# Performance work log

Hardware: AMD Instinct MI355X
Metric: run time of the kernel (lower is better)

The kernel has to match this reference:

```python
import jax, jax.numpy as jnp
import numpy as np
import math

E = 2048; H = 16; NOPE = 128; ROPE = 64; VH = 128; C = 512; QR = 1536
DR = 2; BASE = 10000.0; LR = 4  # hypernet low_rank -> C//4 = 128
B = 2; S = 2048


def _ln(x, g, b):
    m = jnp.mean(x, axis=-1, keepdims=True)
    v = jnp.mean((x - m) ** 2, axis=-1, keepdims=True)
    return (x - m) / jnp.sqrt(v + 1e-5) * g + b


def _rope(x, sin, cos):
    # interleaved rotary: x[..., 0::2], x[..., 1::2]
    x1 = x[..., 0::2]
    x2 = x[..., 1::2]
    out = jnp.stack([x1 * cos - x2 * sin, x1 * sin + x2 * cos], axis=-1)
    return out.reshape(x.shape)


def _sincos(pos, dim):
    inv = BASE ** (-jnp.arange(0, dim, 2, dtype=jnp.float32) / dim)
    ang = pos[:, None] * inv  # [S, dim//2]
    return jnp.sin(ang), jnp.cos(ang)


def _pe(T, d):
    # sinusoidal positional encoding [T, d]
    pos = jnp.arange(T, dtype=jnp.float32)[:, None]
    div = jnp.exp(jnp.arange(0, d, 2, dtype=jnp.float32) * (-math.log(10000.0) / d))
    pe = jnp.zeros((T, d))
    pe = pe.at[:, 0::2].set(jnp.sin(pos * div))
    pe = pe.at[:, 1::2].set(jnp.cos(pos * div))
    return pe


def _forward(query, key, value, wq_a, q_ln_g, q_ln_b, wq_b, wkv_a, kv_ln_g,
             kv_ln_b, wkv_b, wo, fc_c_w, fc_c_b, fc_p_w, fc_p_b, pos_scale):
    B_, S_, _ = query.shape
    # LoRA query path
    ql = _ln(query @ wq_a.T, q_ln_g, q_ln_b)                 # [B,S,QR]
    q = (ql @ wq_b.T).reshape(B_, S_, H, NOPE + ROPE)
    q_nope, q_pe = q[..., :NOPE], q[..., NOPE:]
    # positions: start_pos = key_len - 1 (prefill entering incremental path)
    start = S_ - 1
    pos = jnp.arange(start, start + S_, dtype=jnp.float32)
    sin, cos = _sincos(pos, ROPE)                            # [S, ROPE//2]
    q_pe = _rope(q_pe, sin[None, :, None, :], cos[None, :, None, :])
    # KV latent path
    kvf = key @ wkv_a.T                                      # [B,S,C+ROPE]
    kv, k_pe = kvf[..., :C], kvf[..., C:]
    k_pe = _rope(k_pe, sin[None, :, :], cos[None, :, :])     # [B,S,ROPE]
    kvn = _ln(kv, kv_ln_g, kv_ln_b)                          # [B,S,C]
    # HyperNetwork temporal compression: W [B, t, T]
    T = S_
    t = math.ceil(T / DR)
    Cpe = _pe(t, C)                                          # [t, C]
    C2 = Cpe @ fc_c_w.T + fc_c_b                             # [t, C//LR]
    P2 = kvn @ fc_p_w.T + fc_p_b                             # [B,T,C//LR]
    W = jax.nn.sigmoid(jnp.einsum('tr,bTr->btT', C2, P2))    # [B,t,T]
    # chunk mask: compressed slot r gathers tokens in its down_rate chunk
    zm = (jnp.arange(T)[None, :] // DR == jnp.arange(t)[:, None]).astype(kvn.dtype)
    prev_kv = jnp.einsum('btT,bTc->btc', W * zm[None], kvn)  # [B,t,C]
    idx = list(range(DR - 1, T, DR))
    if T - 1 not in idx:
        idx.append(T - 1)
    prev_kpe = k_pe[:, np.array(idx)]                        # [B,t,ROPE]
    # LoRA-absorbed attention
    wkvb = wkv_b.reshape(H, NOPE + VH, C)
    qn = jnp.einsum('bshd,hdc->bshc', q_nope, wkvb[:, :NOPE])
    content = jnp.einsum('bshc,btc->bsht', qn, prev_kv)
    # decoupled (normalized) rope scores
    qpe_n = q_pe / jnp.maximum(jnp.linalg.norm(q_pe, axis=-1, keepdims=True), 1e-12)
    kpe_n = prev_kpe / jnp.maximum(jnp.linalg.norm(prev_kpe, axis=-1, keepdims=True), 1e-12)
    pscore = jnp.einsum('bshr,btr->bsht', qpe_n, kpe_n)
    scores = (content + pos_scale * pscore) * ((NOPE + ROPE) ** -0.5)
    attn = jax.nn.softmax(scores, axis=-1)                   # [B,S,H,t]
    x = jnp.einsum('bsht,btc->bshc', attn, prev_kv)
    x = jnp.einsum('bshc,hdc->bshd', x, wkvb[:, NOPE:])      # value up-proj
    return x.reshape(B_, S_, H * VH) @ wo.T


def setup_inputs() -> dict:
    key = jax.random.key(0)
    ks = jax.random.split(key, 16)
    s = 0.02
    return {
        'query': jax.random.normal(ks[0], (B, S, E), jnp.float32),
        'key': jax.random.normal(ks[1], (B, S, E), jnp.float32),
        'value': jax.random.normal(ks[2], (B, S, E), jnp.float32),
        'wq_a': jax.random.normal(ks[3], (QR, E), jnp.float32) * s,
        'q_ln_g': jnp.ones((QR,), jnp.float32),
        'q_ln_b': jnp.zeros((QR,), jnp.float32),
        'wq_b': jax.random.normal(ks[4], (H * (NOPE + ROPE), QR), jnp.float32) * s,
        'wkv_a': jax.random.normal(ks[5], (C + ROPE, E), jnp.float32) * s,
        'kv_ln_g': jnp.ones((C,), jnp.float32),
        'kv_ln_b': jnp.zeros((C,), jnp.float32),
        'wkv_b': jax.random.normal(ks[6], (H * (NOPE + VH), C), jnp.float32) * s,
        'wo': jax.random.normal(ks[7], (E, H * VH), jnp.float32) * s,
        'fc_c_w': jax.random.normal(ks[8], (C // LR, C), jnp.float32) * s,
        'fc_c_b': jnp.zeros((C // LR,), jnp.float32),
        'fc_p_w': jax.random.normal(ks[9], (C // LR, C), jnp.float32) * s,
        'fc_p_b': jnp.zeros((C // LR,), jnp.float32),
        'pos_scale': jnp.asarray(1.0, jnp.float32),
    }


def reference(query, key, value, wq_a, q_ln_g, q_ln_b, wq_b, wkv_a, kv_ln_g,
              kv_ln_b, wkv_b, wo, fc_c_w, fc_c_b, fc_p_w, fc_p_b, pos_scale):
    return _forward(query, key, value, wq_a, q_ln_g, q_ln_b, wq_b, wkv_a,
                    kv_ln_g, kv_ln_b, wkv_b, wo, fc_c_w, fc_c_b, fc_p_w,
                    fc_p_b, pos_scale)
```

## Files before the change

### kernel.cpp

```cpp
#include <hip/hip_runtime.h>
#include <math.h>

#define S_ 2048
#define B_ 2
#define H_ 16
#define E_ 2048
#define QR_ 1536
#define NOPE_ 128
#define ROPE_ 64
#define C_ 512
#define VH_ 128
#define T_ 1024
#define LN1E4 9.210340371976184f
#define SCALE_ 0.07216878364870323f

typedef _Float16 half8 __attribute__((ext_vector_type(8)));
typedef _Float16 half4 __attribute__((ext_vector_type(4)));
typedef __fp16 fp16x2 __attribute__((ext_vector_type(2)));
typedef float floatx4 __attribute__((ext_vector_type(4)));
#define MFMA16(a, b, c) __builtin_amdgcn_mfma_f32_16x16x32_f16(a, b, c, 0, 0, 0)

__device__ __forceinline__ void gload16(const _Float16* g, _Float16* l) {
  __builtin_amdgcn_global_load_lds(
      (__attribute__((address_space(1))) const void*)g,
      (__attribute__((address_space(3))) void*)l, 16, 0, 0);
}

__device__ __forceinline__ int xcd_swizzle(int orig, int nwg) {
  int q8 = nwg >> 3, r8 = nwg & 7, xcd = orig & 7, base = orig >> 3;
  return (xcd < r8 ? xcd * (q8 + 1) : r8 * (q8 + 1) + (xcd - r8) * q8) + base;
}

__global__ __launch_bounds__(256) void conv_all(
    const float* __restrict__ q, const float* __restrict__ k,
    const float* __restrict__ wqa, const float* __restrict__ wqb,
    const float* __restrict__ wkva, const float* __restrict__ wo,
    const float* __restrict__ fcc, const float* __restrict__ fcp,
    _Float16* q16, _Float16* k16, _Float16* wqa16, _Float16* wqb16,
    _Float16* wkva16, _Float16* wo16, _Float16* fcc16, _Float16* fcp16)
{
  size_t i = (size_t)blockIdx.x * 256 + threadIdx.x;
  const float* in; _Float16* out; size_t off;
  if      (i < 1048576) { in = q;    out = q16;    off = i; }
  else if (i < 2097152) { in = k;    out = k16;    off = i - 1048576; }
  else if (i < 2490368) { in = wqa;  out = wqa16;  off = i - 2097152; }
  else if (i < 3080192) { in = wqb;  out = wqb16;  off = i - 2490368; }
  else if (i < 3227648) { in = wkva; out = wkva16; off = i - 3080192; }
  else if (i < 3751936) { in = wo;   out = wo16;   off = i - 3227648; }
  else if (i < 3760128) { in = fcc;  out = fcc16;  off = i - 3751936; }
  else                  { in = fcp;  out = fcp16;  off = i - 3760128; }
  float4 a = ((const float4*)in)[2 * off];
  float4 b = ((const float4*)in)[2 * off + 1];
  half8 h = {(_Float16)a.x, (_Float16)a.y, (_Float16)a.z, (_Float16)a.w,
             (_Float16)b.x, (_Float16)b.y, (_Float16)b.z, (_Float16)b.w};
  *(half8*)(out + 8 * off) = h;
}

template<bool OUT16, bool NB, bool BIAS, bool TRANSC>
__global__ __launch_bounds__(256) void gemm16(
    const _Float16* __restrict__ A, const _Float16* __restrict__ Bm,
    const float* __restrict__ bias, float* __restrict__ Cf,
    _Float16* __restrict__ Ch, int N, int K, int lda, int ldb, int ldc,
    long sAb, long sAh, long sBb, long sBh, long sCb, long sCh)
{
  __shared__ __align__(16) _Float16 Asl[2][128 * 64];
  __shared__ __align__(16) _Float16 Bsl[2][128 * 64];
  const int z = blockIdx.z, zb = z >> 4, zh = z & 15;
  A  += (size_t)zb * sAb + (size_t)zh * sAh;
  Bm += (size_t)zb * sBb + (size_t)zh * sBh;
  if (OUT16) Ch += (size_t)zb * sCb + (size_t)zh * sCh;
  else       Cf += (size_t)zb * sCb + (size_t)zh * sCh;
  const int gx = gridDim.x;
  const int nwg = gx * gridDim.y;
  const int f = xcd_swizzle(blockIdx.y * gx + blockIdx.x, nwg);
  const int bm = (f / gx) * 128, bn = (f % gx) * 128;
  const int tid = threadIdx.x;
  const int w = tid >> 6, lane = tid & 63, l15 = lane & 15, g = lane >> 4;
  const int wm = (w >> 1) * 64, wn = (w & 1) * 64;
  const int srow = w * 32 + (lane >> 3);
  const int sch  = (lane & 7) ^ (lane >> 3);
  floatx4 acc[4][4];
  #pragma unroll
  for (int i = 0; i < 4; ++i)
    #pragma unroll
    for (int j = 0; j < 4; ++j) acc[i][j] = (floatx4){0.f, 0.f, 0.f, 0.f};

  auto STAGE = [&](int buf, int k0) {
    _Float16* al = &Asl[buf][w * 2048];
    _Float16* bl = &Bsl[buf][w * 2048];
    #pragma unroll
    for (int i = 0; i < 4; ++i)
      gload16(A + (size_t)(bm + srow + i * 8) * lda + k0 + sch * 8, al + i * 512);
    #pragma unroll
    for (int i = 0; i < 4; ++i)
      gload16(Bm + (size_t)(bn + srow + i * 8) * ldb + k0 + sch * 8, bl + i * 512);
  };

  STAGE(0, 0);
  int cur = 0;
  const int nIter = K >> 6;
  for (int it = 0; it < nIter; ++it) {
    const bool pf = (it + 1 < nIter);
    if (pf) STAGE(cur ^ 1, (it + 1) << 6);
    if (pf) asm volatile("s_waitcnt vmcnt(8)" ::: "memory");
    else    asm volatile("s_waitcnt vmcnt(0)" ::: "memory");
    __builtin_amdgcn_sched_barrier(0);
    __builtin_amdgcn_s_barrier();
    __builtin_amdgcn_sched_barrier(0);
    #pragma unroll
    for (int kk = 0; kk < 2; ++kk) {
      half8 af[4], bf[4];
      const int sw = ((kk * 4 + g) ^ (l15 & 7)) * 8;
      #pragma unroll
      for (int i = 0; i < 4; ++i) {
        af[i] = *(const half8*)&Asl[cur][(wm + i * 16 + l15) * 64 + sw];
        bf[i] = *(const half8*)&Bsl[cur][(wn + i * 16 + l15) * 64 + sw];
      }
      #pragma unroll
      for (int i = 0; i < 4; ++i)
        #pragma unroll
        for (int j = 0; j < 4; ++j)
          acc[i][j] = MFMA16(af[i], bf[j], acc[i][j]);
    }
    asm volatile("s_waitcnt lgkmcnt(0)" ::: "memory");
    __builtin_amdgcn_sched_barrier(0);
    __builtin_amdgcn_s_barrier();
    __builtin_amdgcn_sched_barrier(0);
    cur ^= 1;
  }

  if (TRANSC) {
    #pragma unroll
    for (int i = 0; i < 4; ++i)
      #pragma unroll
      for (int j = 0; j < 4; ++j) {
        int row = bm + wm + i * 16 + g * 4;
        int col = bn + wn + j * 16 + l15;
        half4 v = {(_Float16)acc[i][j][0], (_Float16)acc[i][j][1],
                   (_Float16)acc[i][j][2], (_Float16)acc[i][j][3]};
        *(half4*)(Ch + (size_t)col * ldc + row) = v;
      }
  } else {
    #pragma unroll
    for (int i = 0; i < 4; ++i)
      #pragma unroll
      for (int j = 0; j < 4; ++j)
        #pragma unroll
        for (int r = 0; r < 4; ++r) {
          int row = bm + wm + i * 16 + g * 4 + r;
          int col = bn + wn + j * 16 + l15;
          if (!NB || col < N) {
            float v = acc[i][j][r];
            if (BIAS) v += bias[col];
            if (OUT16) Ch[(size_t)row * ldc + col] = (_Float16)v;
            else       Cf[(size_t)row * ldc + col] = v;
          }
        }
  }
}

template<typename TIN, bool OUT16>
__global__ __launch_bounds__(256) void ln_rows(
    const TIN* __restrict__ in, float* __restrict__ outf, _Float16* __restrict__ outh,
    const float* __restrict__ g, const float* __restrict__ bb,
    int L, int ldin, int ldout)
{
  const int row = blockIdx.x;
  const TIN* x = in + (size_t)row * ldin;
  float s = 0.f, s2 = 0.f;
  for (int i = threadIdx.x; i < L; i += 256) {
    float v = (float)x[i]; s += v; s2 += v * v;
  }
  #pragma unroll
  for (int off = 32; off; off >>= 1) {
    s  += __shfl_xor(s, off, 64);
    s2 += __shfl_xor(s2, off, 64);
  }
  __shared__ float rs[4], rs2[4];
  int lane = threadIdx.x & 63, w = threadIdx.x >> 6;
  if (lane == 0) { rs[w] = s; rs2[w] = s2; }
  __syncthreads();
  s  = rs[0] + rs[1] + rs[2] + rs[3];
  s2 = rs2[0] + rs2[1] + rs2[2] + rs2[3];
  float mean = s / L;
  float var = s2 / L - mean * mean;
  float inv = rsqrtf(var + 1e-5f);
  for (int i = threadIdx.x; i < L; i += 256) {
    float v = ((float)x[i] - mean) * inv * g[i] + bb[i];
    if (OUT16) outh[(size_t)row * ldout + i] = (_Float16)v;
    else       outf[(size_t)row * ldout + i] = v;
  }
}

__global__ __launch_bounds__(64) void rope_q16(_Float16* __restrict__ qb,
                                               const float* __restrict__ ps_ptr)
{
  const int idx = blockIdx.x;
  const int h = idx & (H_ - 1);
  const int row = idx >> 4;
  const int s = row & (S_ - 1);
  _Float16* p = qb + (size_t)row * 3072 + h * 192 + NOPE_;
  const int j = threadIdx.x;
  float o1 = 0.f, o2 = 0.f;
  if (j < 32) {
    float invf = expf(-(float)j * (LN1E4 / 32.f));
    float ang = (float)(S_ - 1 + s) * invf;
    float sn, cs; sincosf(ang, &sn, &cs);
    float x1 = (float)p[2 * j], x2 = (float)p[2 * j + 1];
    o1 = x1 * cs - x2 * sn;
    o2 = x1 * sn + x2 * cs;
  }
  float ss = o1 * o1 + o2 * o2;
  #pragma unroll
  for (int off = 32; off; off >>= 1) ss += __shfl_xor(ss, off, 64);
  float inv = ps_ptr[0] * SCALE_ / fmaxf(sqrtf(ss), 1e-12f);
  if (j < 32) {
    p[2 * j]     = (_Float16)(o1 * inv);
    p[2 * j + 1] = (_Float16)(o2 * inv);
  }
}

__global__ __launch_bounds__(64) void rope_k16(
    const _Float16* __restrict__ kvf16, _Float16* __restrict__ keff)
{
  const int t = blockIdx.x, b = blockIdx.y;
  const int srow = 2 * t + 1;
  const _Float16* p = kvf16 + ((size_t)(b * S_ + srow)) * 576 + C_;
  const int j = threadIdx.x;
  float o1 = 0.f, o2 = 0.f;
  if (j < 32) {
    float invf = expf(-(float)j * (LN1E4 / 32.f));
    float ang = (float)(S_ - 1 + srow) * invf;
    float sn, cs; sincosf(ang, &sn, &cs);
    float x1 = (float)p[2 * j], x2 = (float)p[2 * j + 1];
    o1 = x1 * cs - x2 * sn;
    o2 = x1 * sn + x2 * cs;
  }
  float ss = o1 * o1 + o2 * o2;
  #pragma unroll
  for (int off = 32; off; off >>= 1) ss += __shfl_xor(ss, off, 64);
  float nrm = fmaxf(sqrtf(ss), 1e-12f);
  if (j < 32) {
    _Float16 h1 = (_Float16)(o1 / nrm), h2 = (_Float16)(o2 / nrm);
    #pragma unroll
    for (int h = 0; h < H_; ++h) {
      _Float16* o = keff + ((size_t)((b * H_ + h) * T_) + t) * 192 + NOPE_;
      o[2 * j] = h1; o[2 * j + 1] = h2;
    }
  }
}

__global__ __launch_bounds__(256) void pe16(_Float16* __restrict__ Cpe16)
{
  const int t = blockIdx.x;
  const int i = threadIdx.x;
  float dv = expf(-(float)(2 * i) * (LN1E4 / 512.f));
  float ang = (float)t * dv;
  float sn, cs; sincosf(ang, &sn, &cs);
  Cpe16[(size_t)t * C_ + 2 * i]     = (_Float16)sn;
  Cpe16[(size_t)t * C_ + 2 * i + 1] = (_Float16)cs;
}

__global__ __launch_bounds__(64) void gate_kernel(
    const _Float16* __restrict__ C2, const _Float16* __restrict__ P2,
    const _Float16* __restrict__ kvn16, _Float16* __restrict__ pkv16)
{
  const int t = blockIdx.x, b = blockIdx.y;
  const int j = threadIdx.x;
  const _Float16* c2 = C2 + (size_t)t * 128;
  const _Float16* p0 = P2 + ((size_t)(b * S_ + 2 * t)) * 128;
  const _Float16* p1 = p0 + 128;
  float d0 = (float)c2[j] * (float)p0[j] + (float)c2[j + 64] * (float)p0[j + 64];
  float d1 = (float)c2[j] * (float)p1[j] + (float)c2[j + 64] * (float)p1[j + 64];
  #pragma unroll
  for (int off = 32; off; off >>= 1) {
    d0 += __shfl_xor(d0, off, 64);
    d1 += __shfl_xor(d1, off, 64);
  }
  float w0 = 1.f / (1.f + expf(-d0));
  float w1 = 1.f / (1.f + expf(-d1));
  const _Float16* k0 = kvn16 + ((size_t)(b * S_ + 2 * t)) * C_;
  const _Float16* k1 = k0 + C_;
  _Float16* o = pkv16 + ((size_t)(b * T_ + t)) * C_;
  #pragma unroll
  for (int it = 0; it < 2; ++it) {
    int c = j * 4 + it * 256;
    #pragma unroll
    for (int u = 0; u < 4; ++u)
      o[c + u] = (_Float16)(w0 * (float)k0[c + u] + w1 * (float)k1[c + u]);
  }
}

__global__ __launch_bounds__(256) void conv_wkvb(
    const float* __restrict__ wkvb, _Float16* __restrict__ W1c,
    _Float16* __restrict__ W2c)
{
  int i = blockIdx.x * 256 + threadIdx.x;
  const int half = 16 * 128 * 512;
  if (i < half) {
    int c = i & 511, d = (i >> 9) & 127, h = i >> 16;
    W1c[i] = (_Float16)(wkvb[((size_t)(h * 256 + d)) * 512 + c] * SCALE_);
  } else {
    int j = i - half;
    int c = j & 511, d = (j >> 9) & 127, h = j >> 16;
    W2c[j] = (_Float16)wkvb[((size_t)(h * 256 + 128 + d)) * 512 + c];
  }
}

__global__ __launch_bounds__(256, 3) void attn_flash(
    const _Float16* __restrict__ qb16, const _Float16* __restrict__ keff,
    const _Float16* __restrict__ vT, _Float16* __restrict__ x216)
{
  __shared__ __align__(16) _Float16 K_lds[64 * 200];
  __shared__ __align__(16) _Float16 V_lds[128 * 72];
  const int f = xcd_swizzle(blockIdx.x, 1024);
  const int st = f & 31, h = (f >> 5) & 15, b = f >> 9;
  const int tid = threadIdx.x, w = tid >> 6, lane = tid & 63;
  const int l15 = lane & 15, g = lane >> 4;
  const int rq = b * S_ + st * 64 + w * 16;
  const _Float16* qrow = qb16 + (size_t)(rq + l15) * 3072 + h * 192;
  half8 qB[6];
  #pragma unroll
  for (int kk = 0; kk < 6; ++kk) qB[kk] = *(const half8*)(qrow + kk * 32 + g * 8);
  floatx4 O[8];
  #pragma unroll
  for (int i = 0; i < 8; ++i) O[i] = (floatx4){0.f, 0.f, 0.f, 0.f};
  float m = -3e38f, l = 0.f;
  const _Float16* kb = keff + (size_t)(b * H_ + h) * T_ * 192;
  const _Float16* vb = vT   + (size_t)(b * H_ + h) * 128 * T_;

  const int krow[6] = {(tid) / 24, (tid + 256) / 24, (tid + 512) / 24,
                       (tid + 768) / 24, (tid + 1024) / 24, (tid + 1280) / 24};
  const int kcol[6] = {(tid % 24) * 8, ((tid + 256) % 24) * 8, ((tid + 512) % 24) * 8,
                       ((tid + 768) % 24) * 8, ((tid + 1024) % 24) * 8, ((tid + 1280) % 24) * 8};
  half8 kreg[6], vreg[4];

  #pragma unroll
  for (int p = 0; p < 6; ++p)
    kreg[p] = *(const half8*)(kb + (size_t)krow[p] * 192 + kcol[p]);
  #pragma unroll
  for (int p = 0; p < 4; ++p) {
    int c = tid + p * 256;
    vreg[p] = *(const half8*)(vb + (size_t)(c >> 3) * T_ + (c & 7) * 8);
  }
  #pragma unroll
  for (int p = 0; p < 6; ++p)
    *(half8*)&K_lds[krow[p] * 200 + kcol[p]] = kreg[p];
  #pragma unroll
  for (int p = 0; p < 4; ++p) {
    int c = tid + p * 256;
    *(half8*)&V_lds[(c >> 3) * 72 + (c & 7) * 8] = vreg[p];
  }
  __syncthreads();

  const int srcA = l15 + ((g & 1) << 5);
  const int srcB = srcA + 16;
  const bool hi = (g >> 1) != 0;

  for (int kt = 0; kt < 16; ++kt) {
    if (kt < 15) {
      const int t1 = (kt + 1) * 64;
      #pragma unroll
      for (int p = 0; p < 6; ++p)
        kreg[p] = *(const half8*)(kb + (size_t)(t1 + krow[p]) * 192 + kcol[p]);
      #pragma unroll
      for (int p = 0; p < 4; ++p) {
        int c = tid + p * 256;
        vreg[p] = *(const half8*)(vb + (size_t)(c >> 3) * T_ + t1 + (c & 7) * 8);
      }
    }
    floatx4 sc[4];
    #pragma unroll
    for (int i = 0; i < 4; ++i) sc[i] = (floatx4){0.f, 0.f, 0.f, 0.f};
    __builtin_amdgcn_s_setprio(1);
    #pragma unroll
    for (int kk = 0; kk < 6; ++kk)
      #pragma unroll
      for (int ct = 0; ct < 4; ++ct)
        sc[ct] = MFMA16(
            *(const half8*)&K_lds[(ct * 16 + l15) * 200 + kk * 32 + g * 8],
            qB[kk], sc[ct]);
    __builtin_amdgcn_s_setprio(0);
    float pm = sc[0][0];
    #pragma unroll
    for (int ct = 0; ct < 4; ++ct)
      #pragma unroll
      for (int r = 0; r < 4; ++r) pm = fmaxf(pm, sc[ct][r]);
    pm = fmaxf(pm, __shfl_xor(pm, 16, 64));
    pm = fmaxf(pm, __shfl_xor(pm, 32, 64));
    int ok = pm <= m + 8.f;
    if (!__all(ok)) {
      float mn = fmaxf(m, pm);
      float sf = __expf(m - mn);
      m = mn; l *= sf;
      float sfO[4];
      #pragma unroll
      for (int r = 0; r < 4; ++r) sfO[r] = __shfl(sf, g * 4 + r, 64);
      #pragma unroll
      for (int cc = 0; cc < 8; ++cc) {
        O[cc][0] *= sfO[0]; O[cc][1] *= sfO[1];
        O[cc][2] *= sfO[2]; O[cc][3] *= sfO[3];
      }
    }
    float rs = 0.f;
    #pragma unroll
    for (int ct = 0; ct < 4; ++ct)
      #pragma unroll
      for (int r = 0; r < 4; ++r) {
        float e = __expf(sc[ct][r] - m);
        sc[ct][r] = e; rs += e;
      }
    rs += __shfl_xor(rs, 16, 64);
    rs += __shfl_xor(rs, 32, 64);
    l += rs;
    unsigned pk[4][2];
    #pragma unroll
    for (int ct = 0; ct < 4; ++ct) {
      union { fp16x2 h; unsigned u; } c0, c1;
      c0.h = __builtin_amdgcn_cvt_pkrtz(sc[ct][0], sc[ct][1]);
      c1.h = __builtin_amdgcn_cvt_pkrtz(sc[ct][2], sc[ct][3]);
      pk[ct][0] = c0.u; pk[ct][1] = c1.u;
    }
    __builtin_amdgcn_s_setprio(1);
    #pragma unroll
    for (int kc = 0; kc < 2; ++kc) {
      unsigned a0 = __shfl((int)pk[2 * kc][0], srcA, 64);
      unsigned b0 = __shfl((int)pk[2 * kc + 1][0], srcA, 64);
      unsigned a1 = __shfl((int)pk[2 * kc][1], srcA, 64);
      unsigned b1 = __shfl((int)pk[2 * kc + 1][1], srcA, 64);
      unsigned a2 = __shfl((int)pk[2 * kc][0], srcB, 64);
      unsigned b2 = __shfl((int)pk[2 * kc + 1][0], srcB, 64);
      unsigned a3 = __shfl((int)pk[2 * kc][1], srcB, 64);
      unsigned b3 = __shfl((int)pk[2 * kc + 1][1], srcB, 64);
      union { unsigned u[4]; half8 h; } pa;
      pa.u[0] = hi ? b0 : a0;
      pa.u[1] = hi ? b1 : a1;
      pa.u[2] = hi ? b2 : a2;
      pa.u[3] = hi ? b3 : a3;
      #pragma unroll
      for (int cc = 0; cc < 8; ++cc)
        O[cc] = MFMA16(pa.h,
            *(const half8*)&V_lds[(cc * 16 + l15) * 72 + kc * 32 + g * 8], O[cc]);
    }
    __builtin_amdgcn_s_setprio(0);
    if (kt < 15) {
      __syncthreads();
      #pragma unroll
      for (int p = 0; p < 6; ++p)
        *(half8*)&K_lds[krow[p] * 200 + kcol[p]] = kreg[p];
      #pragma unroll
      for (int p = 0; p < 4; ++p) {
        int c = tid + p * 256;
        *(half8*)&V_lds[(c >> 3) * 72 + (c & 7) * 8] = vreg[p];
      }
      __syncthreads();
    }
  }
  float il = 1.f / l;
  float ilO[4];
  #pragma unroll
  for (int r = 0; r < 4; ++r) ilO[r] = __shfl(il, g * 4 + r, 64);
  #pragma unroll
  for (int cc = 0; cc < 8; ++cc)
    #pragma unroll
    for (int r = 0; r < 4; ++r)
      x216[(size_t)(rq + g * 4 + r) * 2048 + h * 128 + cc * 16 + l15] =
          (_Float16)(O[cc][r] * ilO[r]);
}

extern "C" void kernel_launch(void* const* d_in, const int* in_sizes, int n_in,
                              void* d_out, int out_size, void* d_ws, size_t ws_size,
                              hipStream_t stream)
{
  (void)in_sizes; (void)n_in; (void)out_size; (void)ws_size;
  const float* query  = (const float*)d_in[0];
  const float* key    = (const float*)d_in[1];
  const float* wq_a   = (const float*)d_in[3];
  const float* q_ln_g = (const float*)d_in[4];
  const float* q_ln_b = (const float*)d_in[5];
  const float* wq_b   = (const float*)d_in[6];
  const float* wkv_a  = (const float*)d_in[7];
  const float* kv_ln_g= (const float*)d_in[8];
  const float* kv_ln_b= (const float*)d_in[9];
  const float* wkvb   = (const float*)d_in[10];
  const float* wo     = (const float*)d_in[11];
  const float* fc_c_w = (const float*)d_in[12];
  const float* fc_c_b = (const float*)d_in[13];
  const float* fc_p_w = (const float*)d_in[14];
  const float* fc_p_b = (const float*)d_in[15];
  const float* ps     = (const float*)d_in[16];
  float* out = (float*)d_out;

  const int M = B_ * S_;
  _Float16* hws   = (_Float16*)d_ws;
  _Float16* q16   = hws;
  _Float16* key16 = q16   + (size_t)8388608;
  _Float16* wqa16 = key16 + (size_t)8388608;
  _Float16* wqb16 = wqa16 + (size_t)3145728;
  _Float16* wkva16= wqb16 + (size_t)4718592;
  _Float16* wo16  = wkva16+ (size_t)1179648;
  _Float16* ql16  = wo16  + (size_t)4194304;
  _Float16* qb16  = ql16  + (size_t)6291456;
  _Float16* kvf16 = qb16  + (size_t)12582912;
  _Float16* kvn16 = kvf16 + (size_t)2359296;
  _Float16* fcc16 = kvn16 + (size_t)2097152;
  _Float16* fcp16 = fcc16 + (size_t)65536;
  _Float16* x216  = q16;
  _Float16* keff  = key16;
  _Float16* W1c   = wqa16;
  _Float16* W2c   = W1c + (size_t)1048576;
  _Float16* Cpe16 = wqb16;
  _Float16* C2h   = Cpe16 + (size_t)T_ * C_;
  _Float16* P2h   = C2h + (size_t)T_ * 128;
  _Float16* pkv16 = wkva16;
  _Float16* vT    = ql16;
  float*    qlp   = out;

  conv_all<<<14720, 256, 0, stream>>>(query, key, wq_a, wq_b, wkv_a, wo, fc_c_w, fc_p_w,
                                      q16, key16, wqa16, wqb16, wkva16, wo16, fcc16, fcp16);
  gemm16<false,false,false,false><<<dim3(QR_/128, M/128), 256, 0, stream>>>(
      q16, wqa16, nullptr, qlp, nullptr, QR_, E_, E_, E_, QR_, 0,0,0,0,0,0);
  conv_wkvb<<<8192, 256, 0, stream>>>(wkvb, W1c, W2c);
  ln_rows<float,true><<<M, 256, 0, stream>>>(qlp, nullptr, ql16, q_ln_g, q_ln_b,
                                             QR_, QR_, QR_);
  gemm16<true,false,false,false><<<dim3(3072/128, M/128), 256, 0, stream>>>(
      ql16, wqb16, nullptr, nullptr, qb16, 3072, QR_, QR_, QR_, 3072, 0,0,0,0,0,0);
  rope_q16<<<M * H_, 64, 0, stream>>>(qb16, ps);
  gemm16<true,true,false,false><<<dim3(5, M/128), 256, 0, stream>>>(
      key16, wkva16, nullptr, nullptr, kvf16, 576, E_, E_, E_, 576, 0,0,0,0,0,0);
  ln_rows<_Float16,true><<<M, 256, 0, stream>>>(kvf16, nullptr, kvn16, kv_ln_g, kv_ln_b,
                                                C_, 576, C_);
  rope_k16<<<dim3(T_, B_), 64, 0, stream>>>(kvf16, keff);
  pe16<<<T_, 256, 0, stream>>>(Cpe16);
  gemm16<true,false,true,false><<<dim3(1, T_/128), 256, 0, stream>>>(
      Cpe16, fcc16, fc_c_b, nullptr, C2h, 128, C_, C_, C_, 128, 0,0,0,0,0,0);
  gemm16<true,false,true,false><<<dim3(1, M/128), 256, 0, stream>>>(
      kvn16, fcp16, fc_p_b, nullptr, P2h, 128, C_, C_, C_, 128, 0,0,0,0,0,0);
  gate_kernel<<<dim3(T_, B_), 64, 0, stream>>>(C2h, P2h, kvn16, pkv16);
  gemm16<true,false,false,false><<<dim3(1, T_/128, 32), 256, 0, stream>>>(
      pkv16, W1c, nullptr, nullptr, keff, 128, C_, C_, C_, 192,
      (long)T_*C_, 0L, 0L, (long)128*C_, (long)H_*T_*192, (long)T_*192);
  gemm16<true,false,false,true><<<dim3(1, T_/128, 32), 256, 0, stream>>>(
      pkv16, W2c, nullptr, nullptr, vT, 128, C_, C_, C_, T_,
      (long)T_*C_, 0L, 0L, (long)128*C_, (long)H_*128*T_, (long)128*T_);
  attn_flash<<<dim3(1024), 256, 0, stream>>>(qb16, keff, vT, x216);
  gemm16<false,false,false,false><<<dim3(E_/128, M/128), 256, 0, stream>>>(
      x216, wo16, nullptr, out, nullptr, E_, E_, E_, E_, E_, 0,0,0,0,0,0);
}
```

Before: 379.0 us.

## Fold wkv_b conversion into conv_all and XOR-swizzle attention LDS tiles

The separate scalar conv_wkvb kernel goes away. Its work now runs inside conv_all as vectorized 8-wide conversions into dedicated workspace buffers, which removes one launch and the uncoalesced scalar stores. The attention kernel drops its padded K/V shared-memory layout in favour of an XOR swizzle. This shrinks LDS per block, and launch bounds are raised to allow 4 blocks per CU. The risks are higher register pressure under the tighter occupancy bound, and a possible change in bank-conflict behaviour.

```diff
diff --git a/kernel.cpp b/kernel.cpp
--- a/kernel.cpp
+++ b/kernel.cpp
@@ -36,10 +36,27 @@
     const float* __restrict__ wqa, const float* __restrict__ wqb,
     const float* __restrict__ wkva, const float* __restrict__ wo,
     const float* __restrict__ fcc, const float* __restrict__ fcp,
+    const float* __restrict__ wkvb,
     _Float16* q16, _Float16* k16, _Float16* wqa16, _Float16* wqb16,
-    _Float16* wkva16, _Float16* wo16, _Float16* fcc16, _Float16* fcp16)
+    _Float16* wkva16, _Float16* wo16, _Float16* fcc16, _Float16* fcp16,
+    _Float16* W1c, _Float16* W2c)
 {
   size_t i = (size_t)blockIdx.x * 256 + threadIdx.x;
+  if (i >= 3768320) {
+    bool isW1 = i < 3899392;
+    size_t j = i - (isW1 ? 3768320 : 3899392);
+    int cch = j & 63, hd = (int)(j >> 6);
+    int hh = hd >> 7, dd = hd & 127;
+    const float* src = wkvb + ((size_t)(hh * 256 + (isW1 ? 0 : 128) + dd)) * 512 + cch * 8;
+    float sc = isW1 ? SCALE_ : 1.f;
+    float4 a = *(const float4*)src;
+    float4 b = *(const float4*)(src + 4);
+    half8 h = {(_Float16)(a.x * sc), (_Float16)(a.y * sc), (_Float16)(a.z * sc),
+               (_Float16)(a.w * sc), (_Float16)(b.x * sc), (_Float16)(b.y * sc),
+               (_Float16)(b.z * sc), (_Float16)(b.w * sc)};
+    *(half8*)((isW1 ? W1c : W2c) + j * 8) = h;
+    return;
+  }
   const float* in; _Float16* out; size_t off;
   if      (i < 1048576) { in = q;    out = q16;    off = i; }
   else if (i < 2097152) { in = k;    out = k16;    off = i - 1048576; }
@@ -291,32 +308,16 @@
   }
 }
 
-__global__ __launch_bounds__(256) void conv_wkvb(
-    const float* __restrict__ wkvb, _Float16* __restrict__ W1c,
-    _Float16* __restrict__ W2c)
-{
-  int i = blockIdx.x * 256 + threadIdx.x;
-  const int half = 16 * 128 * 512;
-  if (i < half) {
-    int c = i & 511, d = (i >> 9) & 127, h = i >> 16;
-    W1c[i] = (_Float16)(wkvb[((size_t)(h * 256 + d)) * 512 + c] * SCALE_);
-  } else {
-    int j = i - half;
-    int c = j & 511, d = (j >> 9) & 127, h = j >> 16;
-    W2c[j] = (_Float16)wkvb[((size_t)(h * 256 + 128 + d)) * 512 + c];
-  }
-}
-
-__global__ __launch_bounds__(256, 3) void attn_flash(
+__global__ __launch_bounds__(256, 4) void attn_flash(
     const _Float16* __restrict__ qb16, const _Float16* __restrict__ keff,
     const _Float16* __restrict__ vT, _Float16* __restrict__ x216)
 {
-  __shared__ __align__(16) _Float16 K_lds[64 * 200];
-  __shared__ __align__(16) _Float16 V_lds[128 * 72];
+  __shared__ __align__(16) _Float16 K_lds[64 * 192];
+  __shared__ __align__(16) _Float16 V_lds[128 * 64];
   const int f = xcd_swizzle(blockIdx.x, 1024);
   const int st = f & 31, h = (f >> 5) & 15, b = f >> 9;
   const int tid = threadIdx.x, w = tid >> 6, lane = tid & 63;
-  const int l15 = lane & 15, g = lane >> 4;
+  const int l15 = lane & 15, g = lane >> 4, l7 = lane & 7;
   const int rq = b * S_ + st * 64 + w * 16;
   const _Float16* qrow = qb16 + (size_t)(rq + l15) * 3072 + h * 192;
   half8 qB[6];
@@ -329,28 +330,36 @@
   const _Float16* kb = keff + (size_t)(b * H_ + h) * T_ * 192;
   const _Float16* vb = vT   + (size_t)(b * H_ + h) * 128 * T_;
 
-  const int krow[6] = {(tid) / 24, (tid + 256) / 24, (tid + 512) / 24,
-                       (tid + 768) / 24, (tid + 1024) / 24, (tid + 1280) / 24};
-  const int kcol[6] = {(tid % 24) * 8, ((tid + 256) % 24) * 8, ((tid + 512) % 24) * 8,
-                       ((tid + 768) % 24) * 8, ((tid + 1024) % 24) * 8, ((tid + 1280) % 24) * 8};
-  half8 kreg[6], vreg[4];
-
-  #pragma unroll
-  for (int p = 0; p < 6; ++p)
-    kreg[p] = *(const half8*)(kb + (size_t)krow[p] * 192 + kcol[p]);
+  int ksrc[6], ksw[6], vsrc[4], vsw[4];
+  #pragma unroll
+  for (int p = 0; p < 6; ++p) {
+    int c = tid + p * 256;
+    int r = c / 24, dc = c % 24;
+    ksrc[p] = r * 192 + dc * 8;
+    ksw[p]  = r * 192 + ((dc ^ (r & 7)) * 8);
+  }
   #pragma unroll
   for (int p = 0; p < 4; ++p) {
     int c = tid + p * 256;
-    vreg[p] = *(const half8*)(vb + (size_t)(c >> 3) * T_ + (c & 7) * 8);
-  }
-  #pragma unroll
-  for (int p = 0; p < 6; ++p)
-    *(half8*)&K_lds[krow[p] * 200 + kcol[p]] = kreg[p];
-  #pragma unroll
-  for (int p = 0; p < 4; ++p) {
-    int c = tid + p * 256;
-    *(half8*)&V_lds[(c >> 3) * 72 + (c & 7) * 8] = vreg[p];
-  }
+    int r = c >> 3, dc = c & 7;
+    vsrc[p] = r * T_ + dc * 8;
+    vsw[p]  = r * 64 + ((dc ^ (r & 7)) * 8);
+  }
+  int kswr[6], vswr[2];
+  #pragma unroll
+  for (int kk = 0; kk < 6; ++kk) kswr[kk] = ((kk * 4 + g) ^ l7) * 8;
+  #pragma unroll
+  for (int kc = 0; kc < 2; ++kc) vswr[kc] = ((kc * 4 + g) ^ l7) * 8;
+
+  half8 kreg[6], vreg[4];
+  #pragma unroll
+  for (int p = 0; p < 6; ++p) kreg[p] = *(const half8*)(kb + ksrc[p]);
+  #pragma unroll
+  for (int p = 0; p < 4; ++p) vreg[p] = *(const half8*)(vb + vsrc[p]);
+  #pragma unroll
+  for (int p = 0; p < 6; ++p) *(half8*)&K_lds[ksw[p]] = kreg[p];
+  #pragma unroll
+  for (int p = 0; p < 4; ++p) *(half8*)&V_lds[vsw[p]] = vreg[p];
   __syncthreads();
 
   const int srcA = l15 + ((g & 1) << 5);
@@ -362,12 +371,10 @@
       const int t1 = (kt + 1) * 64;
       #pragma unroll
       for (int p = 0; p < 6; ++p)
-        kreg[p] = *(const half8*)(kb + (size_t)(t1 + krow[p]) * 192 + kcol[p]);
-      #pragma unroll
-      for (int p = 0; p < 4; ++p) {
-        int c = tid + p * 256;
-        vreg[p] = *(const half8*)(vb + (size_t)(c >> 3) * T_ + t1 + (c & 7) * 8);
-      }
+        kreg[p] = *(const half8*)(kb + (size_t)t1 * 192 + ksrc[p]);
+      #pragma unroll
+      for (int p = 0; p < 4; ++p)
+        vreg[p] = *(const half8*)(vb + t1 + vsrc[p]);
     }
     floatx4 sc[4];
     #pragma unroll
@@ -378,7 +385,7 @@
       #pragma unroll
       for (int ct = 0; ct < 4; ++ct)
         sc[ct] = MFMA16(
-            *(const half8*)&K_lds[(ct * 16 + l15) * 200 + kk * 32 + g * 8],
+            *(const half8*)&K_lds[(ct * 16 + l15) * 192 + kswr[kk]],
             qB[kk], sc[ct]);
     __builtin_amdgcn_s_setprio(0);
     float pm = sc[0][0];
@@ -440,19 +447,15 @@
       #pragma unroll
       for (int cc = 0; cc < 8; ++cc)
         O[cc] = MFMA16(pa.h,
-            *(const half8*)&V_lds[(cc * 16 + l15) * 72 + kc * 32 + g * 8], O[cc]);
+            *(const half8*)&V_lds[(cc * 16 + l15) * 64 + vswr[kc]], O[cc]);
     }
     __builtin_amdgcn_s_setprio(0);
     if (kt < 15) {
       __syncthreads();
       #pragma unroll
-      for (int p = 0; p < 6; ++p)
-        *(half8*)&K_lds[krow[p] * 200 + kcol[p]] = kreg[p];
-      #pragma unroll
-      for (int p = 0; p < 4; ++p) {
-        int c = tid + p * 256;
-        *(half8*)&V_lds[(c >> 3) * 72 + (c & 7) * 8] = vreg[p];
-      }
+      for (int p = 0; p < 6; ++p) *(half8*)&K_lds[ksw[p]] = kreg[p];
+      #pragma unroll
+      for (int p = 0; p < 4; ++p) *(half8*)&V_lds[vsw[p]] = vreg[p];
       __syncthreads();
     }
   }
@@ -505,10 +508,10 @@
   _Float16* kvn16 = kvf16 + (size_t)2359296;
   _Float16* fcc16 = kvn16 + (size_t)2097152;
   _Float16* fcp16 = fcc16 + (size_t)65536;
+  _Float16* W1c   = fcp16 + (size_t)65536;
+  _Float16* W2c   = W1c   + (size_t)1048576;
   _Float16* x216  = q16;
   _Float16* keff  = key16;
-  _Float16* W1c   = wqa16;
-  _Float16* W2c   = W1c + (size_t)1048576;
   _Float16* Cpe16 = wqb16;
   _Float16* C2h   = Cpe16 + (size_t)T_ * C_;
   _Float16* P2h   = C2h + (size_t)T_ * 128;
@@ -516,11 +519,11 @@
   _Float16* vT    = ql16;
   float*    qlp   = out;
 
-  conv_all<<<14720, 256, 0, stream>>>(query, key, wq_a, wq_b, wkv_a, wo, fc_c_w, fc_p_w,
-                                      q16, key16, wqa16, wqb16, wkva16, wo16, fcc16, fcp16);
+  conv_all<<<15744, 256, 0, stream>>>(query, key, wq_a, wq_b, wkv_a, wo, fc_c_w, fc_p_w,
+                                      wkvb, q16, key16, wqa16, wqb16, wkva16, wo16,
+                                      fcc16, fcp16, W1c, W2c);
   gemm16<false,false,false,false><<<dim3(QR_/128, M/128), 256, 0, stream>>>(
       q16, wqa16, nullptr, qlp, nullptr, QR_, E_, E_, E_, QR_, 0,0,0,0,0,0);
-  conv_wkvb<<<8192, 256, 0, stream>>>(wkvb, W1c, W2c);
   ln_rows<float,true><<<M, 256, 0, stream>>>(qlp, nullptr, ql16, q_ln_g, q_ln_b,
                                              QR_, QR_, QR_);
   gemm16<true,false,false,false><<<dim3(3072/128, M/128), 256, 0, stream>>>(
```

After: 447.5 us. +18.1%, slower.
